# Kernel optimization log

Hardware: AMD Instinct MI355X
Metric: run time of the kernel (lower is better)

The kernel has to match this reference:

```python
import jax, jax.numpy as jnp
import numpy as np

D_OUT, D_IN, NOBJ, H, A = 12, 2, 8, 256, 100
BN_EPS = 1e-5
N_TOK = 16384  # = 2048 scenes * 8 objects


def _lin(x, W, b=None):
    y = x @ W.T
    return y + b if b is not None else y


def _bn1(x, gamma, beta):
    # BatchNorm1d(num_features=1) in training mode: single channel ->
    # batch statistics are taken over every element of the tensor.
    m = jnp.mean(x)
    v = jnp.var(x)
    return (x - m) * (gamma / jnp.sqrt(v + BN_EPS)) + beta


def _l2norm(x):
    # torch.nn.functional.normalize(dim=-1): x / max(||x||, 1e-12)
    n = jnp.linalg.norm(x, axis=-1, keepdims=True)
    return x / jnp.maximum(n, 1e-12)


def setup_inputs() -> dict:
    key = jax.random.key(0)
    ks = iter(jax.random.split(key, 64))
    def rn(shape, s=1.0):
        return jax.random.normal(next(ks), shape, dtype=jnp.float32) * s
    dx = 2 * (D_OUT + D_IN)       # 28
    df = 2 * (D_OUT + 1 + D_IN)   # 30
    p = 0.05
    return dict(
        z_dyn=rn((N_TOK, D_IN)),
        z_contex=rn((N_TOK, D_OUT)),
        z_mc=rn((N_TOK, 2)),
        W_e=rn((H, dx), p), b_e=rn((H,), p),      # linear_inter
        W_i=rn((H, df), p), b_i=rn((H,), p),      # linear_inter_i
        W_a=rn((H, dx), p), b_a=rn((H,), p),      # linear_inter_a
        W_2=rn((H, H), p), b_2=rn((H,), p),       # linear_inter_2
        W_at=rn((A, H), p), b_at=rn((A,), p),     # linear_att
        W_at2=rn((1, A), p), b_at2=rn((1,), p),   # linear_att_2
        W_s1=rn((H, H), p), b_s1=rn((H,), p),     # linear_S[0]
        W_s2=rn((1, H), p), b_s2=rn((1,), p),     # linear_S[1]
        W_eC=rn((H, df), p), b_eC=rn((H,), p),    # linear_inter_C
        W_iC=rn((H, df), p), b_iC=rn((H,), p),    # linear_inter_i_C
        W_2C=rn((H, H), p), b_2C=rn((H,), p),     # linear_inter_2_C
        W_s1C=rn((H, H), p), b_s1C=rn((H,), p),   # linear_S_C[0]
        W_s2C=rn((1, H), p), b_s2C=rn((1,), p),   # linear_S_C[1]
        g_M=jnp.ones((1,), jnp.float32), be_M=jnp.zeros((1,), jnp.float32),
        g_C=jnp.ones((1,), jnp.float32), be_C=jnp.zeros((1,), jnp.float32),
        W_d=rn((D_IN, H), p),   # dynamic_update (no bias)
        W_dC=rn((D_IN, H), p),  # dynamic_update_C (no bias)
    )


def reference(z_dyn, z_contex, z_mc,
              W_e, b_e, W_i, b_i, W_a, b_a, W_2, b_2,
              W_at, b_at, W_at2, b_at2, W_s1, b_s1, W_s2, b_s2,
              W_eC, b_eC, W_iC, b_iC, W_2C, b_2C,
              W_s1C, b_s1C, W_s2C, b_s2C,
              g_M, be_M, g_C, be_C, W_d, W_dC):
    B = z_dyn.shape[0] // NOBJ
    cd = jnp.concatenate([z_dyn, z_contex], -1).reshape(B, NOBJ, D_IN + D_OUT)
    zm = z_mc[:, 0].reshape(B, NOBJ, 1)
    zc = z_mc[:, 1].reshape(B, NOBJ, 1)
    v = z_dyn.reshape(B, NOBJ, D_IN)
    ct = z_contex.reshape(B, NOBJ, D_OUT)

    def pair(a):
        d = a.shape[-1]
        a1 = jnp.broadcast_to(a[:, None, :, :], (B, NOBJ, NOBJ, d))  # [b,i,j] = a[b,j]
        a2 = jnp.broadcast_to(a[:, :, None, :], (B, NOBJ, NOBJ, d))  # [b,i,j] = a[b,i]
        return a1, a2

    x1, x2 = pair(cd)
    m1, m2 = pair(zm)
    v1, v2 = pair(v)
    ct1, ct2 = pair(ct)
    c1, c2 = pair(zc)

    x_12 = jnp.concatenate([x1, x2], -1)                       # (B,8,8,28)
    f_12 = jnp.concatenate([m1, x1, m2, x2], -1)               # (B,8,8,30)
    fc_12 = jnp.concatenate([ct1, ct2, c1, c2, v1, v2], -1)    # (B,8,8,30)

    E_emb = jax.nn.relu(_lin(x_12, W_e, b_e))
    I_emb = jax.nn.relu(_lin(f_12, W_i, b_i))
    A_emb = jax.nn.relu(_lin(x_12, W_a, b_a))
    E_embC = jax.nn.relu(_lin(fc_12, W_eC, b_eC))
    I_embC = jax.nn.relu(_lin(fc_12, W_iC, b_iC))
    # NOTE: linear_inter_a_C / linear_att_C / linear_att_2_C (presents_C) are
    # dead code in the original forward (computed but never used) -> omitted.

    presents = jax.nn.sigmoid(
        _lin(jnp.tanh(_lin(A_emb, W_at, b_at)), W_at2, b_at2))  # (B,8,8,1)
    mask = (1.0 - jnp.eye(NOBJ, dtype=x_12.dtype))[None, :, :, None]
    pm = presents * mask

    s = _lin(_lin(I_emb, W_s1, b_s1), W_s2, b_s2)               # (B,8,8,1)
    normed = _bn1(s, g_M, be_M)
    scale = (jax.nn.softplus(normed) * pm).sum(axis=1).reshape(B * NOBJ, 1)

    sC = _lin(_lin(I_embC, W_s1C, b_s1C), W_s2C, b_s2C)
    normedC = _bn1(sC, g_C, be_C)
    scaleC = (jax.nn.softplus(normedC) * mask).sum(axis=1).reshape(B * NOBJ, 1)

    E = (_lin(E_emb, W_2, b_2) * pm).sum(axis=1)                # (B,8,256)
    E_C = (_lin(E_embC, W_2C, b_2C) * mask).sum(axis=1)         # (B,8,256)

    nd_mass = scale * _l2norm(_lin(E, W_d).reshape(z_dyn.shape))
    nd_charge = scaleC * _l2norm(_lin(E_C, W_dC).reshape(z_dyn.shape))
    return (nd_mass + nd_charge, nd_mass, nd_charge)
```

## Files before the change

### kernel.cpp

```cpp
#include <hip/hip_runtime.h>
#include <math.h>

#define HDIM 256
#define NATT 100
#define NPAD 112

typedef __attribute__((ext_vector_type(8))) short short8v;
typedef __attribute__((ext_vector_type(4))) float f32x4;

static __device__ __forceinline__ unsigned short f2bf(float x) {
    union { float f; unsigned u; } v; v.f = x;
    const unsigned r = v.u + 0x7FFFu + ((v.u >> 16) & 1u);
    return (unsigned short)(r >> 16);
}
static __device__ __forceinline__ float bf2f(unsigned short s) {
    union { float f; unsigned u; } v; v.u = ((unsigned)s) << 16;
    return v.f;
}

__launch_bounds__(256)
__global__ void prep_kernel(
    const float* __restrict__ Ws1, const float* __restrict__ bs1,
    const float* __restrict__ Ws2, const float* __restrict__ bs2,
    const float* __restrict__ Ws1C, const float* __restrict__ bs1C,
    const float* __restrict__ Ws2C, const float* __restrict__ bs2C,
    const float* __restrict__ W2,  const float* __restrict__ b2,
    const float* __restrict__ Wd,
    const float* __restrict__ W2C, const float* __restrict__ b2C,
    const float* __restrict__ WdC,
    const float* __restrict__ W_at,
    float* __restrict__ wcm, float* __restrict__ wcc,
    float* __restrict__ m2m, float* __restrict__ m2c,
    float* __restrict__ consts,
    unsigned short* __restrict__ Wh, unsigned short* __restrict__ Wl)
{
    const int h = threadIdx.x;
    const int blk = blockIdx.x;
    if (blk == 0) {
        float a = 0.f;
        for (int k = 0; k < HDIM; ++k) a += Ws2[k] * Ws1[k*HDIM + h];
        wcm[h] = a;
        if (h == 0) {
            float bsum = bs2[0];
            for (int k = 0; k < HDIM; ++k) bsum += Ws2[k] * bs1[k];
            consts[0] = bsum;
        }
    } else if (blk == 1) {
        float a = 0.f;
        for (int k = 0; k < HDIM; ++k) a += Ws2C[k] * Ws1C[k*HDIM + h];
        wcc[h] = a;
        if (h == 0) {
            float bsum = bs2C[0];
            for (int k = 0; k < HDIM; ++k) bsum += Ws2C[k] * bs1C[k];
            consts[1] = bsum;
        }
    } else if (blk < 4) {
        const int c = blk - 2;
        float a = 0.f;
        for (int k = 0; k < HDIM; ++k) a += Wd[c*HDIM + k] * W2[k*HDIM + h];
        m2m[c*HDIM + h] = a;
        if (h == 0) {
            float bsum = 0.f;
            for (int k = 0; k < HDIM; ++k) bsum += Wd[c*HDIM + k] * b2[k];
            consts[2 + c] = bsum;
        }
    } else if (blk < 6) {
        const int c = blk - 4;
        float a = 0.f;
        for (int k = 0; k < HDIM; ++k) a += WdC[c*HDIM + k] * W2C[k*HDIM + h];
        m2c[c*HDIM + h] = a;
        if (h == 0) {
            float bsum = 0.f;
            for (int k = 0; k < HDIM; ++k) bsum += WdC[c*HDIM + k] * b2C[k];
            consts[4 + c] = bsum;
        }
    } else {
        const int rbase = (blk - 6) * 14;
        for (int rr = 0; rr < 14; ++rr) {
            const int row = rbase + rr;
            const float v = (row < NATT) ? W_at[row*HDIM + h] : 0.f;
            const unsigned short hi = f2bf(v);
            Wh[row*HDIM + h] = hi;
            Wl[row*HDIM + h] = f2bf(v - bf2f(hi));
        }
    }
}

__launch_bounds__(256, 4)
__global__ void main_kernel(
    const float* __restrict__ z_dyn, const float* __restrict__ z_contex,
    const float* __restrict__ z_mc,
    const float* __restrict__ W_e,  const float* __restrict__ b_e,
    const float* __restrict__ W_i,  const float* __restrict__ b_i,
    const float* __restrict__ W_a,  const float* __restrict__ b_a,
    const float* __restrict__ b_at,
    const float* __restrict__ W_at2,const float* __restrict__ b_at2,
    const float* __restrict__ W_eC, const float* __restrict__ b_eC,
    const float* __restrict__ W_iC, const float* __restrict__ b_iC,
    const unsigned short* __restrict__ Wh, const unsigned short* __restrict__ Wl,
    const float* __restrict__ wcm,  const float* __restrict__ wcc,
    const float* __restrict__ m2m,  const float* __restrict__ m2c,
    const float* __restrict__ consts,
    float* __restrict__ pm_g, float* __restrict__ s_g, float* __restrict__ sC_g,
    float* __restrict__ um_g, float* __restrict__ uc_g, float* __restrict__ part_g)
{
    __shared__ float s_in[8][16];
    alignas(16) __shared__ float proj[16][260];
    alignas(16) __shared__ float AccE[8][260];
    alignas(16) __shared__ float AccC[8][260];
    __shared__ float pm_t[64];
    __shared__ float pmsum_s[8];
    __shared__ float ss_s[64];
    __shared__ float sc_s[64];
    __shared__ float y_s[32];

    const int tid = threadIdx.x;
    const int b = blockIdx.x;

    if (tid < 128) {
        const int o = tid >> 4, c = tid & 15;
        const int tok = b*8 + o;
        float v;
        if (c < 2)       v = z_dyn[tok*2 + c];
        else if (c < 14) v = z_contex[tok*12 + (c-2)];
        else             v = z_mc[tok*2 + (c-14)];
        s_in[o][c] = v;
    }
    __syncthreads();

    {
        const int h = tid;
        float w[28];
        #pragma unroll
        for (int k = 0; k < 28; ++k) w[k] = W_a[h*28 + k];
        const float hb = 0.5f * b_a[h];
        #pragma unroll
        for (int o = 0; o < 8; ++o) {
            float pj = hb, pi = hb;
            #pragma unroll
            for (int k = 0; k < 14; ++k) {
                const float x = s_in[o][k];
                pj += w[k]    * x;
                pi += w[14+k] * x;
            }
            proj[o][h]   = pj;
            proj[8+o][h] = pi;
        }
    }
    __syncthreads();

    {
        const int w    = tid >> 6;
        const int lane = tid & 63;
        const int lr   = lane & 15;
        const int lk   = lane >> 4;
        const int pA = 16*w + lr;
        const int jA = pA & 7, iA = pA >> 3;

        f32x4 acc[7];
        #pragma unroll
        for (int n = 0; n < 7; ++n) acc[n] = (f32x4){0.f, 0.f, 0.f, 0.f};

        #pragma unroll 2
        for (int k = 0; k < 8; ++k) {
            const int kb = k*32 + lk*8;
            const float4 vj0 = *(const float4*)&proj[jA][kb];
            const float4 vj1 = *(const float4*)&proj[jA][kb+4];
            const float4 vi0 = *(const float4*)&proj[8+iA][kb];
            const float4 vi1 = *(const float4*)&proj[8+iA][kb+4];
            float v[8] = {vj0.x+vi0.x, vj0.y+vi0.y, vj0.z+vi0.z, vj0.w+vi0.w,
                          vj1.x+vi1.x, vj1.y+vi1.y, vj1.z+vi1.z, vj1.w+vi1.w};
            short8v ah, al;
            #pragma unroll
            for (int e = 0; e < 8; ++e) {
                const float r = fmaxf(v[e], 0.f);
                const unsigned short h16 = f2bf(r);
                ah[e] = (short)h16;
                al[e] = (short)f2bf(r - bf2f(h16));
            }
            #pragma unroll
            for (int n = 0; n < 7; ++n) {
                const int a = 16*n + lr;
                const short8v bh = *(const short8v*)&Wh[a*HDIM + kb];
                const short8v bl = *(const short8v*)&Wl[a*HDIM + kb];
                acc[n] = __builtin_amdgcn_mfma_f32_16x16x32_bf16(ah, bh, acc[n], 0, 0, 0);
                acc[n] = __builtin_amdgcn_mfma_f32_16x16x32_bf16(al, bh, acc[n], 0, 0, 0);
                acc[n] = __builtin_amdgcn_mfma_f32_16x16x32_bf16(ah, bl, acc[n], 0, 0, 0);
            }
        }

        float part[4] = {0.f, 0.f, 0.f, 0.f};
        #pragma unroll
        for (int n = 0; n < 7; ++n) {
            const int a = 16*n + lr;
            if (a < NATT) {
                const float bat = b_at[a], wat2 = W_at2[a];
                #pragma unroll
                for (int r = 0; r < 4; ++r)
                    part[r] += wat2 * tanhf(acc[n][r] + bat);
            }
        }
        #pragma unroll
        for (int r = 0; r < 4; ++r) {
            float s = part[r];
            s += __shfl_xor(s, 1); s += __shfl_xor(s, 2);
            s += __shfl_xor(s, 4); s += __shfl_xor(s, 8);
            part[r] = s;
        }
        if (lr == 0) {
            const float b2v = b_at2[0];
            #pragma unroll
            for (int r = 0; r < 4; ++r) {
                const int p = 16*w + 4*lk + r;
                const int ip = p >> 3, jp = p & 7;
                const float pres = 1.f / (1.f + expf(-(part[r] + b2v)));
                const float pmv = (ip != jp) ? pres : 0.f;
                pm_t[jp*8 + ip] = pmv;
                pm_g[b*64 + jp*8 + ip] = pmv;
            }
        }
    }
    __syncthreads();

    if (tid < 8) {
        float su = 0.f;
        #pragma unroll
        for (int i = 0; i < 8; ++i) su += pm_t[tid*8 + i];
        pmsum_s[tid] = su;
    }

    {
        const int h = tid;
        float w[30];
        #pragma unroll
        for (int k = 0; k < 30; ++k) w[k] = W_i[h*30 + k];
        const float hb = 0.5f * b_i[h];
        #pragma unroll
        for (int o = 0; o < 8; ++o) {
            const float zm = s_in[o][14];
            float pj = hb + w[0]*zm, pi = hb + w[15]*zm;
            #pragma unroll
            for (int k = 0; k < 14; ++k) {
                const float x = s_in[o][k];
                pj += w[1+k]  * x;
                pi += w[16+k] * x;
            }
            proj[o][h]   = pj;
            proj[8+o][h] = pi;
        }
    }
    __syncthreads();
    {
        const int p = tid >> 2, l2 = tid & 3;
        const int ip = p >> 3, jp = p & 7;
        float a = 0.f;
        #pragma unroll
        for (int u = 0; u < 16; ++u) {
            const int h4 = (l2*16 + u) * 4;
            const float4 aj = *(const float4*)&proj[jp][h4];
            const float4 ai = *(const float4*)&proj[8+ip][h4];
            const float4 wv = *(const float4*)&wcm[h4];
            a += wv.x*fmaxf(aj.x+ai.x, 0.f) + wv.y*fmaxf(aj.y+ai.y, 0.f)
               + wv.z*fmaxf(aj.z+ai.z, 0.f) + wv.w*fmaxf(aj.w+ai.w, 0.f);
        }
        a += __shfl_xor(a, 1); a += __shfl_xor(a, 2);
        if (l2 == 0) {
            const float sv = a + consts[0];
            ss_s[p] = sv;
            s_g[b*64 + jp*8 + ip] = sv;
        }
    }
    __syncthreads();

    {
        const int h = tid;
        float w[30];
        #pragma unroll
        for (int k = 0; k < 30; ++k) w[k] = W_iC[h*30 + k];
        const float hb = 0.5f * b_iC[h];
        #pragma unroll
        for (int o = 0; o < 8; ++o) {
            const float zc = s_in[o][15];
            const float v0 = s_in[o][0], v1 = s_in[o][1];
            float pj = hb + w[24]*zc + w[26]*v0 + w[27]*v1;
            float pi = hb + w[25]*zc + w[28]*v0 + w[29]*v1;
            #pragma unroll
            for (int k = 0; k < 12; ++k) {
                const float x = s_in[o][2+k];
                pj += w[k]    * x;
                pi += w[12+k] * x;
            }
            proj[o][h]   = pj;
            proj[8+o][h] = pi;
        }
    }
    __syncthreads();
    {
        const int p = tid >> 2, l2 = tid & 3;
        const int ip = p >> 3, jp = p & 7;
        float a = 0.f;
        #pragma unroll
        for (int u = 0; u < 16; ++u) {
            const int h4 = (l2*16 + u) * 4;
            const float4 aj = *(const float4*)&proj[jp][h4];
            const float4 ai = *(const float4*)&proj[8+ip][h4];
            const float4 wv = *(const float4*)&wcc[h4];
            a += wv.x*fmaxf(aj.x+ai.x, 0.f) + wv.y*fmaxf(aj.y+ai.y, 0.f)
               + wv.z*fmaxf(aj.z+ai.z, 0.f) + wv.w*fmaxf(aj.w+ai.w, 0.f);
        }
        a += __shfl_xor(a, 1); a += __shfl_xor(a, 2);
        if (l2 == 0) {
            const float sv = a + consts[1];
            sc_s[p] = sv;
            sC_g[b*64 + jp*8 + ip] = sv;
        }
    }
    __syncthreads();

    if (tid < 64) {
        const float v1 = ss_s[tid], v2 = sc_s[tid];
        float a0 = v1, a1 = v1*v1, a2 = v2, a3 = v2*v2;
        #pragma unroll
        for (int m = 1; m < 64; m <<= 1) {
            a0 += __shfl_xor(a0, m); a1 += __shfl_xor(a1, m);
            a2 += __shfl_xor(a2, m); a3 += __shfl_xor(a3, m);
        }
        if (tid == 0) {
            part_g[b*4 + 0] = a0; part_g[b*4 + 1] = a1;
            part_g[b*4 + 2] = a2; part_g[b*4 + 3] = a3;
        }
    }

    {
        const int h = tid;
        float w[28];
        #pragma unroll
        for (int k = 0; k < 28; ++k) w[k] = W_e[h*28 + k];
        const float hb = 0.5f * b_e[h];
        #pragma unroll
        for (int o = 0; o < 8; ++o) {
            float pj = hb, pi = hb;
            #pragma unroll
            for (int k = 0; k < 14; ++k) {
                const float x = s_in[o][k];
                pj += w[k]    * x;
                pi += w[14+k] * x;
            }
            proj[o][h]   = pj;
            proj[8+o][h] = pi;
        }
    }
    __syncthreads();
    {
        const int h = tid;
        float Pj[8], Pi[8];
        #pragma unroll
        for (int o = 0; o < 8; ++o) { Pj[o] = proj[o][h]; Pi[o] = proj[8+o][h]; }
        #pragma unroll
        for (int j = 0; j < 8; ++j) {
            const float4 pm0 = *(const float4*)&pm_t[j*8];
            const float4 pm1 = *(const float4*)&pm_t[j*8 + 4];
            const float pjv = Pj[j];
            float a = pm0.x*fmaxf(pjv+Pi[0],0.f) + pm0.y*fmaxf(pjv+Pi[1],0.f)
                    + pm0.z*fmaxf(pjv+Pi[2],0.f) + pm0.w*fmaxf(pjv+Pi[3],0.f)
                    + pm1.x*fmaxf(pjv+Pi[4],0.f) + pm1.y*fmaxf(pjv+Pi[5],0.f)
                    + pm1.z*fmaxf(pjv+Pi[6],0.f) + pm1.w*fmaxf(pjv+Pi[7],0.f);
            AccE[j][h] = a;
        }
    }
    __syncthreads();

    {
        const int h = tid;
        float w[30];
        #pragma unroll
        for (int k = 0; k < 30; ++k) w[k] = W_eC[h*30 + k];
        const float hb = 0.5f * b_eC[h];
        #pragma unroll
        for (int o = 0; o < 8; ++o) {
            const float zc = s_in[o][15];
            const float v0 = s_in[o][0], v1 = s_in[o][1];
            float pj = hb + w[24]*zc + w[26]*v0 + w[27]*v1;
            float pi = hb + w[25]*zc + w[28]*v0 + w[29]*v1;
            #pragma unroll
            for (int k = 0; k < 12; ++k) {
                const float x = s_in[o][2+k];
                pj += w[k]    * x;
                pi += w[12+k] * x;
            }
            proj[o][h]   = pj;
            proj[8+o][h] = pi;
        }
    }
    __syncthreads();
    {
        const int h = tid;
        float Pj[8], Pi[8];
        #pragma unroll
        for (int o = 0; o < 8; ++o) { Pj[o] = proj[o][h]; Pi[o] = proj[8+o][h]; }
        #pragma unroll
        for (int j = 0; j < 8; ++j) {
            const float pjv = Pj[j];
            float a = 0.f;
            #pragma unroll
            for (int i = 0; i < 8; ++i)
                a += (i != j) ? fmaxf(pjv + Pi[i], 0.f) : 0.f;
            AccC[j][h] = a;
        }
    }
    __syncthreads();

    {
        const int t = tid >> 3, l3 = tid & 7;
        const int type = t >> 4, c = (t >> 3) & 1, jj = t & 7;
        const float* M2 = type ? m2c : m2m;
        const float (*Acc)[260] = type ? AccC : AccE;
        float a = 0.f;
        #pragma unroll
        for (int u = 0; u < 8; ++u) {
            const int h4 = l3*32 + u*4;
            const float4 mv = *(const float4*)&M2[c*256 + h4];
            const float4 av = *(const float4*)&Acc[jj][h4];
            a += mv.x*av.x + mv.y*av.y + mv.z*av.z + mv.w*av.w;
        }
        a += __shfl_xor(a, 1); a += __shfl_xor(a, 2); a += __shfl_xor(a, 4);
        if (l3 == 0) {
            const float bd = consts[2 + type*2 + c];
            const float pms = type ? 7.0f : pmsum_s[jj];
            y_s[t] = a + pms * bd;
        }
    }
    __syncthreads();
    if (tid < 16) {
        const int type = tid >> 3, j = tid & 7;
        const float y0 = y_s[type*16 + j];
        const float y1 = y_s[type*16 + 8 + j];
        const float n = fmaxf(sqrtf(y0*y0 + y1*y1), 1e-12f);
        float* u = type ? uc_g : um_g;
        u[(b*8 + j)*2 + 0] = y0 / n;
        u[(b*8 + j)*2 + 1] = y1 / n;
    }
}

__launch_bounds__(256)
__global__ void stats_kernel(const float* __restrict__ part,
                             const float* __restrict__ gM, const float* __restrict__ beM,
                             const float* __restrict__ gC, const float* __restrict__ beC,
                             float* __restrict__ stats, int nblk, float inv_n)
{
    __shared__ float red[4][4];
    float a0 = 0.f, a1 = 0.f, a2 = 0.f, a3 = 0.f;
    for (int r = threadIdx.x; r < nblk; r += 256) {
        const float4 v = ((const float4*)part)[r];
        a0 += v.x; a1 += v.y; a2 += v.z; a3 += v.w;
    }
    #pragma unroll
    for (int m = 1; m < 64; m <<= 1) {
        a0 += __shfl_xor(a0, m); a1 += __shfl_xor(a1, m);
        a2 += __shfl_xor(a2, m); a3 += __shfl_xor(a3, m);
    }
    const int w = threadIdx.x >> 6;
    if ((threadIdx.x & 63) == 0) {
        red[0][w] = a0; red[1][w] = a1; red[2][w] = a2; red[3][w] = a3;
    }
    __syncthreads();
    if (threadIdx.x == 0) {
        float s = 0.f, s2 = 0.f, sc = 0.f, sc2 = 0.f;
        for (int k = 0; k < 4; ++k) {
            s += red[0][k]; s2 += red[1][k]; sc += red[2][k]; sc2 += red[3][k];
        }
        float mean = s * inv_n;
        float var  = s2 * inv_n - mean*mean;
        float kk   = gM[0] / sqrtf(var + 1e-5f);
        stats[0] = kk;
        stats[1] = beM[0] - mean*kk;
        mean = sc * inv_n;
        var  = sc2 * inv_n - mean*mean;
        kk   = gC[0] / sqrtf(var + 1e-5f);
        stats[2] = kk;
        stats[3] = beC[0] - mean*kk;
    }
}

__launch_bounds__(256)
__global__ void final_kernel(const float* __restrict__ s_g, const float* __restrict__ sC_g,
                             const float* __restrict__ pm_g,
                             const float* __restrict__ um_g, const float* __restrict__ uc_g,
                             const float* __restrict__ stats,
                             float* __restrict__ out, int ntok)
{
    const int t = blockIdx.x * blockDim.x + threadIdx.x;
    if (t >= ntok) return;
    const int j = t & 7;
    const float kM = stats[0], cM = stats[1], kC = stats[2], cC = stats[3];
    const float4 sa = *(const float4*)&s_g[t*8];
    const float4 sb = *(const float4*)&s_g[t*8 + 4];
    const float4 ca = *(const float4*)&sC_g[t*8];
    const float4 cb = *(const float4*)&sC_g[t*8 + 4];
    const float4 pa = *(const float4*)&pm_g[t*8];
    const float4 pb = *(const float4*)&pm_g[t*8 + 4];
    const float sv[8] = {sa.x,sa.y,sa.z,sa.w, sb.x,sb.y,sb.z,sb.w};
    const float cv[8] = {ca.x,ca.y,ca.z,ca.w, cb.x,cb.y,cb.z,cb.w};
    const float pv[8] = {pa.x,pa.y,pa.z,pa.w, pb.x,pb.y,pb.z,pb.w};
    float sc = 0.f, scC = 0.f, spj = 0.f;
    #pragma unroll
    for (int i = 0; i < 8; ++i) {
        const float sn = sv[i]*kM + cM;
        const float sp = fmaxf(sn, 0.f) + log1pf(expf(-fabsf(sn)));
        sc += sp * pv[i];
        const float snc = cv[i]*kC + cC;
        const float spc = fmaxf(snc, 0.f) + log1pf(expf(-fabsf(snc)));
        scC += spc;
        if (i == j) spj = spc;
    }
    scC -= spj;
    const float2 u_m = *(const float2*)&um_g[t*2];
    const float2 u_c = *(const float2*)&uc_g[t*2];
    const float m0 = sc  * u_m.x, m1 = sc  * u_m.y;
    const float c0 = scC * u_c.x, c1 = scC * u_c.y;
    *(float2*)&out[t*2]          = make_float2(m0 + c0, m1 + c1);
    *(float2*)&out[ntok*2 + t*2] = make_float2(m0, m1);
    *(float2*)&out[ntok*4 + t*2] = make_float2(c0, c1);
}

extern "C" void kernel_launch(void* const* d_in, const int* in_sizes, int n_in,
                              void* d_out, int out_size, void* d_ws, size_t ws_size,
                              hipStream_t stream) {
    const float* z_dyn    = (const float*)d_in[0];
    const float* z_contex = (const float*)d_in[1];
    const float* z_mc     = (const float*)d_in[2];
    const float* W_e   = (const float*)d_in[3];  const float* b_e   = (const float*)d_in[4];
    const float* W_i   = (const float*)d_in[5];  const float* b_i   = (const float*)d_in[6];
    const float* W_a   = (const float*)d_in[7];  const float* b_a   = (const float*)d_in[8];
    const float* W_2   = (const float*)d_in[9];  const float* b_2   = (const float*)d_in[10];
    const float* W_at  = (const float*)d_in[11]; const float* b_at  = (const float*)d_in[12];
    const float* W_at2 = (const float*)d_in[13]; const float* b_at2 = (const float*)d_in[14];
    const float* W_s1  = (const float*)d_in[15]; const float* b_s1  = (const float*)d_in[16];
    const float* W_s2  = (const float*)d_in[17]; const float* b_s2  = (const float*)d_in[18];
    const float* W_eC  = (const float*)d_in[19]; const float* b_eC  = (const float*)d_in[20];
    const float* W_iC  = (const float*)d_in[21]; const float* b_iC  = (const float*)d_in[22];
    const float* W_2C  = (const float*)d_in[23]; const float* b_2C  = (const float*)d_in[24];
    const float* W_s1C = (const float*)d_in[25]; const float* b_s1C = (const float*)d_in[26];
    const float* W_s2C = (const float*)d_in[27]; const float* b_s2C = (const float*)d_in[28];
    const float* g_M   = (const float*)d_in[29]; const float* be_M  = (const float*)d_in[30];
    const float* g_C   = (const float*)d_in[31]; const float* be_C  = (const float*)d_in[32];
    const float* W_d   = (const float*)d_in[33];
    const float* W_dC  = (const float*)d_in[34];

    const int ntok = in_sizes[0] / 2;
    const int B = ntok / 8;

    float* ws = (float*)d_ws;
    float* pm_g   = ws;
    float* s_g    = pm_g + B*64;
    float* sC_g   = s_g  + B*64;
    float* um_g   = sC_g + B*64;
    float* uc_g   = um_g + ntok*2;
    float* part_g = uc_g + ntok*2;
    float* wcm    = part_g + B*4;
    float* wcc    = wcm + 256;
    float* m2m    = wcc + 256;
    float* m2c    = m2m + 512;
    float* consts = m2c + 512;
    float* stats  = consts + 8;
    unsigned short* Wh = (unsigned short*)(stats + 4);
    unsigned short* Wl = Wh + NPAD*HDIM;

    prep_kernel<<<14, 256, 0, stream>>>(
        W_s1, b_s1, W_s2, b_s2, W_s1C, b_s1C, W_s2C, b_s2C,
        W_2, b_2, W_d, W_2C, b_2C, W_dC, W_at,
        wcm, wcc, m2m, m2c, consts, Wh, Wl);

    main_kernel<<<B, 256, 0, stream>>>(
        z_dyn, z_contex, z_mc,
        W_e, b_e, W_i, b_i, W_a, b_a, b_at, W_at2, b_at2,
        W_eC, b_eC, W_iC, b_iC,
        Wh, Wl,
        wcm, wcc, m2m, m2c, consts,
        pm_g, s_g, sC_g, um_g, uc_g, part_g);

    stats_kernel<<<1, 256, 0, stream>>>(
        part_g, g_M, be_M, g_C, be_C, stats, B, 1.0f / (float)(B*64));

    final_kernel<<<(ntok + 255)/256, 256, 0, stream>>>(
        s_g, sC_g, pm_g, um_g, uc_g, stats, (float*)d_out, ntok);
}
```

Before: 353.7 us.

## Move per-object input projections onto split-bf16 MFMA and drop stats kernel

The five per-object input projections (W_a, W_i, W_iC, W_e, W_eC) were computed with scalar FMAs per thread. They now run as bf16 MFMA tiles. The weights are pre-packed in the prep kernel into hi/lo bf16 pairs with the bias folded in as an extra column, and inputs are split into hi/lo bf16 as well. The separate single-block stats kernel is replaced by per-block atomic adds into a global accumulator, and the final kernel derives the BN coefficients itself. This removes scalar ALU work and one launch, at the cost of split-bf16 precision (three MFMAs per tile) and float atomics, which make accumulation order non-deterministic.

```diff
diff --git a/kernel.cpp b/kernel.cpp
--- a/kernel.cpp
+++ b/kernel.cpp
@@ -4,6 +4,7 @@
 #define HDIM 256
 #define NATT 100
 #define NPAD 112
+#define PSTR 260
 
 typedef __attribute__((ext_vector_type(8))) short short8v;
 typedef __attribute__((ext_vector_type(4))) float f32x4;
@@ -29,10 +30,16 @@
     const float* __restrict__ W2C, const float* __restrict__ b2C,
     const float* __restrict__ WdC,
     const float* __restrict__ W_at,
+    const float* __restrict__ W_a,  const float* __restrict__ b_a,
+    const float* __restrict__ W_i,  const float* __restrict__ b_i,
+    const float* __restrict__ W_iC, const float* __restrict__ b_iC,
+    const float* __restrict__ W_e,  const float* __restrict__ b_e,
+    const float* __restrict__ W_eC, const float* __restrict__ b_eC,
     float* __restrict__ wcm, float* __restrict__ wcc,
     float* __restrict__ m2m, float* __restrict__ m2c,
-    float* __restrict__ consts,
-    unsigned short* __restrict__ Wh, unsigned short* __restrict__ Wl)
+    float* __restrict__ consts, float* __restrict__ stats_acc,
+    unsigned short* __restrict__ Wh, unsigned short* __restrict__ Wl,
+    unsigned short* __restrict__ WcH, unsigned short* __restrict__ WcL)
 {
     const int h = threadIdx.x;
     const int blk = blockIdx.x;
@@ -44,6 +51,8 @@
             float bsum = bs2[0];
             for (int k = 0; k < HDIM; ++k) bsum += Ws2[k] * bs1[k];
             consts[0] = bsum;
+            stats_acc[0] = 0.f; stats_acc[1] = 0.f;
+            stats_acc[2] = 0.f; stats_acc[3] = 0.f;
         }
     } else if (blk == 1) {
         float a = 0.f;
@@ -74,8 +83,43 @@
             for (int k = 0; k < HDIM; ++k) bsum += WdC[c*HDIM + k] * b2C[k];
             consts[4 + c] = bsum;
         }
+    } else if (blk < 16) {
+        const int q = blk - 6;
+        const int m = q >> 1, x = q & 1;
+        const float* W; const float* bias; int type;
+        switch (m) {
+            case 0:  W = W_a;  bias = b_a;  type = 0; break;
+            case 1:  W = W_i;  bias = b_i;  type = 1; break;
+            case 2:  W = W_iC; bias = b_iC; type = 2; break;
+            case 3:  W = W_e;  bias = b_e;  type = 0; break;
+            default: W = W_eC; bias = b_eC; type = 2; break;
+        }
+        float tmp[32];
+        #pragma unroll
+        for (int k = 0; k < 32; ++k) tmp[k] = 0.f;
+        if (type == 0) {
+            const float* row = W + h*28 + x*14;
+            for (int k = 0; k < 14; ++k) tmp[k] = row[k];
+        } else if (type == 1) {
+            const float* row = W + h*30 + x*15;
+            tmp[14] = row[0];
+            for (int k = 0; k < 14; ++k) tmp[k] = row[1+k];
+        } else {
+            const float* row = W + h*30;
+            for (int k = 0; k < 12; ++k) tmp[2+k] = row[x*12 + k];
+            tmp[15] = row[24 + x];
+            tmp[0] = row[26 + x*2];
+            tmp[1] = row[27 + x*2];
+        }
+        tmp[16] = 0.5f * bias[h];
+        const int base = (q*HDIM + h)*32;
+        for (int k = 0; k < 32; ++k) {
+            const unsigned short hi = f2bf(tmp[k]);
+            WcH[base + k] = hi;
+            WcL[base + k] = f2bf(tmp[k] - bf2f(hi));
+        }
     } else {
-        const int rbase = (blk - 6) * 14;
+        const int rbase = (blk - 16) * 14;
         for (int rr = 0; rr < 14; ++rr) {
             const int row = rbase + rr;
             const float v = (row < NATT) ? W_at[row*HDIM + h] : 0.f;
@@ -90,32 +134,33 @@
 __global__ void main_kernel(
     const float* __restrict__ z_dyn, const float* __restrict__ z_contex,
     const float* __restrict__ z_mc,
-    const float* __restrict__ W_e,  const float* __restrict__ b_e,
-    const float* __restrict__ W_i,  const float* __restrict__ b_i,
-    const float* __restrict__ W_a,  const float* __restrict__ b_a,
     const float* __restrict__ b_at,
-    const float* __restrict__ W_at2,const float* __restrict__ b_at2,
-    const float* __restrict__ W_eC, const float* __restrict__ b_eC,
-    const float* __restrict__ W_iC, const float* __restrict__ b_iC,
+    const float* __restrict__ W_at2, const float* __restrict__ b_at2,
     const unsigned short* __restrict__ Wh, const unsigned short* __restrict__ Wl,
+    const unsigned short* __restrict__ WcH, const unsigned short* __restrict__ WcL,
     const float* __restrict__ wcm,  const float* __restrict__ wcc,
     const float* __restrict__ m2m,  const float* __restrict__ m2c,
     const float* __restrict__ consts,
     float* __restrict__ pm_g, float* __restrict__ s_g, float* __restrict__ sC_g,
-    float* __restrict__ um_g, float* __restrict__ uc_g, float* __restrict__ part_g)
+    float* __restrict__ um_g, float* __restrict__ uc_g,
+    float* __restrict__ stats_acc)
 {
     __shared__ float s_in[8][16];
-    alignas(16) __shared__ float proj[16][260];
-    alignas(16) __shared__ float AccE[8][260];
-    alignas(16) __shared__ float AccC[8][260];
+    alignas(16) __shared__ float proj[16][PSTR];
+    alignas(16) __shared__ float AccE[8][PSTR];
+    alignas(16) __shared__ float AccC[8][PSTR];
     __shared__ float pm_t[64];
     __shared__ float pmsum_s[8];
     __shared__ float ss_s[64];
     __shared__ float sc_s[64];
     __shared__ float y_s[32];
 
-    const int tid = threadIdx.x;
-    const int b = blockIdx.x;
+    const int tid  = threadIdx.x;
+    const int b    = blockIdx.x;
+    const int lane = tid & 63;
+    const int lw   = tid >> 6;
+    const int lr   = lane & 15;
+    const int lq   = lane >> 4;
 
     if (tid < 128) {
         const int o = tid >> 4, c = tid & 15;
@@ -128,42 +173,47 @@
     }
     __syncthreads();
 
+    short8v bfh, bfl;
+    #pragma unroll
+    for (int e = 0; e < 8; ++e) {
+        const int k = lq*8 + e;
+        float f = 0.f;
+        if (lr < 8) f = (k < 16) ? s_in[lr][k] : (k == 16 ? 1.0f : 0.f);
+        const unsigned short h16 = f2bf(f);
+        bfh[e] = (short)h16;
+        bfl[e] = (short)f2bf(f - bf2f(h16));
+    }
+
+#define PROJECT(MIDX)                                                          \
+    {                                                                          \
+        const int mb = (MIDX)*2*HDIM*32;                                       \
+        _Pragma("unroll")                                                      \
+        for (int jj = 0; jj < 8; ++jj) {                                       \
+            const int job = lw*8 + jj;                                         \
+            const int x = job >> 4, t = job & 15;                              \
+            const int off = mb + ((x*HDIM) + t*16 + lr)*32 + lq*8;             \
+            const short8v ah = *(const short8v*)&WcH[off];                     \
+            const short8v al = *(const short8v*)&WcL[off];                     \
+            f32x4 d = (f32x4){0.f, 0.f, 0.f, 0.f};                             \
+            d = __builtin_amdgcn_mfma_f32_16x16x32_bf16(ah, bfh, d, 0, 0, 0);  \
+            d = __builtin_amdgcn_mfma_f32_16x16x32_bf16(al, bfh, d, 0, 0, 0);  \
+            d = __builtin_amdgcn_mfma_f32_16x16x32_bf16(ah, bfl, d, 0, 0, 0);  \
+            if (lr < 8) *(f32x4*)&proj[x*8 + lr][t*16 + lq*4] = d;             \
+        }                                                                      \
+    }                                                                          \
+    __syncthreads();
+
+    PROJECT(0)
     {
-        const int h = tid;
-        float w[28];
-        #pragma unroll
-        for (int k = 0; k < 28; ++k) w[k] = W_a[h*28 + k];
-        const float hb = 0.5f * b_a[h];
-        #pragma unroll
-        for (int o = 0; o < 8; ++o) {
-            float pj = hb, pi = hb;
-            #pragma unroll
-            for (int k = 0; k < 14; ++k) {
-                const float x = s_in[o][k];
-                pj += w[k]    * x;
-                pi += w[14+k] * x;
-            }
-            proj[o][h]   = pj;
-            proj[8+o][h] = pi;
-        }
-    }
-    __syncthreads();
-
-    {
-        const int w    = tid >> 6;
-        const int lane = tid & 63;
-        const int lr   = lane & 15;
-        const int lk   = lane >> 4;
-        const int pA = 16*w + lr;
+        const int pA = 16*lw + lr;
         const int jA = pA & 7, iA = pA >> 3;
-
         f32x4 acc[7];
         #pragma unroll
         for (int n = 0; n < 7; ++n) acc[n] = (f32x4){0.f, 0.f, 0.f, 0.f};
 
         #pragma unroll 2
         for (int k = 0; k < 8; ++k) {
-            const int kb = k*32 + lk*8;
+            const int kb = k*32 + lq*8;
             const float4 vj0 = *(const float4*)&proj[jA][kb];
             const float4 vj1 = *(const float4*)&proj[jA][kb+4];
             const float4 vi0 = *(const float4*)&proj[8+iA][kb];
@@ -188,7 +238,6 @@
                 acc[n] = __builtin_amdgcn_mfma_f32_16x16x32_bf16(ah, bl, acc[n], 0, 0, 0);
             }
         }
-
         float part[4] = {0.f, 0.f, 0.f, 0.f};
         #pragma unroll
         for (int n = 0; n < 7; ++n) {
@@ -211,7 +260,7 @@
             const float b2v = b_at2[0];
             #pragma unroll
             for (int r = 0; r < 4; ++r) {
-                const int p = 16*w + 4*lk + r;
+                const int p = 16*lw + 4*lq + r;
                 const int ip = p >> 3, jp = p & 7;
                 const float pres = 1.f / (1.f + expf(-(part[r] + b2v)));
                 const float pmv = (ip != jp) ? pres : 0.f;
@@ -228,28 +277,7 @@
         for (int i = 0; i < 8; ++i) su += pm_t[tid*8 + i];
         pmsum_s[tid] = su;
     }
-
-    {
-        const int h = tid;
-        float w[30];
-        #pragma unroll
-        for (int k = 0; k < 30; ++k) w[k] = W_i[h*30 + k];
-        const float hb = 0.5f * b_i[h];
-        #pragma unroll
-        for (int o = 0; o < 8; ++o) {
-            const float zm = s_in[o][14];
-            float pj = hb + w[0]*zm, pi = hb + w[15]*zm;
-            #pragma unroll
-            for (int k = 0; k < 14; ++k) {
-                const float x = s_in[o][k];
-                pj += w[1+k]  * x;
-                pi += w[16+k] * x;
-            }
-            proj[o][h]   = pj;
-            proj[8+o][h] = pi;
-        }
-    }
-    __syncthreads();
+    PROJECT(1)
     {
         const int p = tid >> 2, l2 = tid & 3;
         const int ip = p >> 3, jp = p & 7;
@@ -272,29 +300,7 @@
     }
     __syncthreads();
 
-    {
-        const int h = tid;
-        float w[30];
-        #pragma unroll
-        for (int k = 0; k < 30; ++k) w[k] = W_iC[h*30 + k];
-        const float hb = 0.5f * b_iC[h];
-        #pragma unroll
-        for (int o = 0; o < 8; ++o) {
-            const float zc = s_in[o][15];
-            const float v0 = s_in[o][0], v1 = s_in[o][1];
-            float pj = hb + w[24]*zc + w[26]*v0 + w[27]*v1;
-            float pi = hb + w[25]*zc + w[28]*v0 + w[29]*v1;
-            #pragma unroll
-            for (int k = 0; k < 12; ++k) {
-                const float x = s_in[o][2+k];
-                pj += w[k]    * x;
-                pi += w[12+k] * x;
-            }
-            proj[o][h]   = pj;
-            proj[8+o][h] = pi;
-        }
-    }
-    __syncthreads();
+    PROJECT(2)
     {
         const int p = tid >> 2, l2 = tid & 3;
         const int ip = p >> 3, jp = p & 7;
@@ -321,36 +327,16 @@
         const float v1 = ss_s[tid], v2 = sc_s[tid];
         float a0 = v1, a1 = v1*v1, a2 = v2, a3 = v2*v2;
         #pragma unroll
-        for (int m = 1; m < 64; m <<= 1) {
-            a0 += __shfl_xor(a0, m); a1 += __shfl_xor(a1, m);
-            a2 += __shfl_xor(a2, m); a3 += __shfl_xor(a3, m);
+        for (int mm = 1; mm < 64; mm <<= 1) {
+            a0 += __shfl_xor(a0, mm); a1 += __shfl_xor(a1, mm);
+            a2 += __shfl_xor(a2, mm); a3 += __shfl_xor(a3, mm);
         }
         if (tid == 0) {
-            part_g[b*4 + 0] = a0; part_g[b*4 + 1] = a1;
-            part_g[b*4 + 2] = a2; part_g[b*4 + 3] = a3;
-        }
-    }
-
-    {
-        const int h = tid;
-        float w[28];
-        #pragma unroll
-        for (int k = 0; k < 28; ++k) w[k] = W_e[h*28 + k];
-        const float hb = 0.5f * b_e[h];
-        #pragma unroll
-        for (int o = 0; o < 8; ++o) {
-            float pj = hb, pi = hb;
-            #pragma unroll
-            for (int k = 0; k < 14; ++k) {
-                const float x = s_in[o][k];
-                pj += w[k]    * x;
-                pi += w[14+k] * x;
-            }
-            proj[o][h]   = pj;
-            proj[8+o][h] = pi;
-        }
-    }
-    __syncthreads();
+            atomicAdd(&stats_acc[0], a0); atomicAdd(&stats_acc[1], a1);
+            atomicAdd(&stats_acc[2], a2); atomicAdd(&stats_acc[3], a3);
+        }
+    }
+    PROJECT(3)
     {
         const int h = tid;
         float Pj[8], Pi[8];
@@ -370,29 +356,7 @@
     }
     __syncthreads();
 
-    {
-        const int h = tid;
-        float w[30];
-        #pragma unroll
-        for (int k = 0; k < 30; ++k) w[k] = W_eC[h*30 + k];
-        const float hb = 0.5f * b_eC[h];
-        #pragma unroll
-        for (int o = 0; o < 8; ++o) {
-            const float zc = s_in[o][15];
-            const float v0 = s_in[o][0], v1 = s_in[o][1];
-            float pj = hb + w[24]*zc + w[26]*v0 + w[27]*v1;
-            float pi = hb + w[25]*zc + w[28]*v0 + w[29]*v1;
-            #pragma unroll
-            for (int k = 0; k < 12; ++k) {
-                const float x = s_in[o][2+k];
-                pj += w[k]    * x;
-                pi += w[12+k] * x;
-            }
-            proj[o][h]   = pj;
-            proj[8+o][h] = pi;
-        }
-    }
-    __syncthreads();
+    PROJECT(4)
     {
         const int h = tid;
         float Pj[8], Pi[8];
@@ -414,7 +378,7 @@
         const int t = tid >> 3, l3 = tid & 7;
         const int type = t >> 4, c = (t >> 3) & 1, jj = t & 7;
         const float* M2 = type ? m2c : m2m;
-        const float (*Acc)[260] = type ? AccC : AccE;
+        const float (*Acc)[PSTR] = type ? AccC : AccE;
         float a = 0.f;
         #pragma unroll
         for (int u = 0; u < 8; ++u) {
@@ -440,59 +404,30 @@
         u[(b*8 + j)*2 + 0] = y0 / n;
         u[(b*8 + j)*2 + 1] = y1 / n;
     }
-}
-
-__launch_bounds__(256)
-__global__ void stats_kernel(const float* __restrict__ part,
-                             const float* __restrict__ gM, const float* __restrict__ beM,
-                             const float* __restrict__ gC, const float* __restrict__ beC,
-                             float* __restrict__ stats, int nblk, float inv_n)
-{
-    __shared__ float red[4][4];
-    float a0 = 0.f, a1 = 0.f, a2 = 0.f, a3 = 0.f;
-    for (int r = threadIdx.x; r < nblk; r += 256) {
-        const float4 v = ((const float4*)part)[r];
-        a0 += v.x; a1 += v.y; a2 += v.z; a3 += v.w;
-    }
-    #pragma unroll
-    for (int m = 1; m < 64; m <<= 1) {
-        a0 += __shfl_xor(a0, m); a1 += __shfl_xor(a1, m);
-        a2 += __shfl_xor(a2, m); a3 += __shfl_xor(a3, m);
-    }
-    const int w = threadIdx.x >> 6;
-    if ((threadIdx.x & 63) == 0) {
-        red[0][w] = a0; red[1][w] = a1; red[2][w] = a2; red[3][w] = a3;
-    }
-    __syncthreads();
-    if (threadIdx.x == 0) {
-        float s = 0.f, s2 = 0.f, sc = 0.f, sc2 = 0.f;
-        for (int k = 0; k < 4; ++k) {
-            s += red[0][k]; s2 += red[1][k]; sc += red[2][k]; sc2 += red[3][k];
-        }
-        float mean = s * inv_n;
-        float var  = s2 * inv_n - mean*mean;
-        float kk   = gM[0] / sqrtf(var + 1e-5f);
-        stats[0] = kk;
-        stats[1] = beM[0] - mean*kk;
-        mean = sc * inv_n;
-        var  = sc2 * inv_n - mean*mean;
-        kk   = gC[0] / sqrtf(var + 1e-5f);
-        stats[2] = kk;
-        stats[3] = beC[0] - mean*kk;
-    }
+#undef PROJECT
 }
 
 __launch_bounds__(256)
 __global__ void final_kernel(const float* __restrict__ s_g, const float* __restrict__ sC_g,
                              const float* __restrict__ pm_g,
                              const float* __restrict__ um_g, const float* __restrict__ uc_g,
-                             const float* __restrict__ stats,
-                             float* __restrict__ out, int ntok)
+                             const float* __restrict__ stats_acc,
+                             const float* __restrict__ gM, const float* __restrict__ beM,
+                             const float* __restrict__ gC, const float* __restrict__ beC,
+                             float* __restrict__ out, int ntok, float inv_n)
 {
     const int t = blockIdx.x * blockDim.x + threadIdx.x;
     if (t >= ntok) return;
     const int j = t & 7;
-    const float kM = stats[0], cM = stats[1], kC = stats[2], cC = stats[3];
+    float mean = stats_acc[0] * inv_n;
+    float var  = stats_acc[1] * inv_n - mean*mean;
+    const float kM = gM[0] / sqrtf(var + 1e-5f);
+    const float cM = beM[0] - mean*kM;
+    mean = stats_acc[2] * inv_n;
+    var  = stats_acc[3] * inv_n - mean*mean;
+    const float kC = gC[0] / sqrtf(var + 1e-5f);
+    const float cC = beC[0] - mean*kC;
+
     const float4 sa = *(const float4*)&s_g[t*8];
     const float4 sb = *(const float4*)&s_g[t*8 + 4];
     const float4 ca = *(const float4*)&sC_g[t*8];
@@ -556,32 +491,32 @@
     float* sC_g   = s_g  + B*64;
     float* um_g   = sC_g + B*64;
     float* uc_g   = um_g + ntok*2;
-    float* part_g = uc_g + ntok*2;
-    float* wcm    = part_g + B*4;
+    float* wcm    = uc_g + ntok*2;
     float* wcc    = wcm + 256;
     float* m2m    = wcc + 256;
     float* m2c    = m2m + 512;
     float* consts = m2c + 512;
-    float* stats  = consts + 8;
-    unsigned short* Wh = (unsigned short*)(stats + 4);
-    unsigned short* Wl = Wh + NPAD*HDIM;
-
-    prep_kernel<<<14, 256, 0, stream>>>(
+    float* stats_acc = consts + 8;
+    unsigned short* Wh  = (unsigned short*)(stats_acc + 4);
+    unsigned short* Wl  = Wh + NPAD*HDIM;
+    unsigned short* WcH = Wl + NPAD*HDIM;
+    unsigned short* WcL = WcH + 10*HDIM*32;
+
+    prep_kernel<<<24, 256, 0, stream>>>(
         W_s1, b_s1, W_s2, b_s2, W_s1C, b_s1C, W_s2C, b_s2C,
         W_2, b_2, W_d, W_2C, b_2C, W_dC, W_at,
-        wcm, wcc, m2m, m2c, consts, Wh, Wl);
+        W_a, b_a, W_i, b_i, W_iC, b_iC, W_e, b_e, W_eC, b_eC,
+        wcm, wcc, m2m, m2c, consts, stats_acc, Wh, Wl, WcH, WcL);
 
     main_kernel<<<B, 256, 0, stream>>>(
         z_dyn, z_contex, z_mc,
-        W_e, b_e, W_i, b_i, W_a, b_a, b_at, W_at2, b_at2,
-        W_eC, b_eC, W_iC, b_iC,
-        Wh, Wl,
+        b_at, W_at2, b_at2,
+        Wh, Wl, WcH, WcL,
         wcm, wcc, m2m, m2c, consts,
-        pm_g, s_g, sC_g, um_g, uc_g, part_g);
-
-    stats_kernel<<<1, 256, 0, stream>>>(
-        part_g, g_M, be_M, g_C, be_C, stats, B, 1.0f / (float)(B*64));
+        pm_g, s_g, sC_g, um_g, uc_g, stats_acc);
 
     final_kernel<<<(ntok + 255)/256, 256, 0, stream>>>(
-        s_g, sC_g, pm_g, um_g, uc_g, stats, (float*)d_out, ntok);
+        s_g, sC_g, pm_g, um_g, uc_g, stats_acc,
+        g_M, be_M, g_C, be_C,
+        (float*)d_out, ntok, 1.0f / (float)(B*64));
 }
```

Result: slower. 446.2 us (+26.2%).
